# Kernel tuning notes

Hardware: AMD Instinct MI355X
Metric: run time of the kernel (lower is better)

## Reference

```python
import jax, jax.numpy as jnp
import numpy as np

# dims: B batch, T timesteps, V nodes, D in-features, C channels, d pos-emb dim,
# TS = t_size (spatio-temporal window), P prediction steps, L layers (=4, fixed by GLU(C*4))
B, T, V, D, C, d, TS, P, L = 4, 12, 512, 1, 64, 8, 3, 12, 4
BETA = TS - 1


def setup_inputs() -> dict:
    key = jax.random.key(0)
    ks = jax.random.split(key, 30)
    n = lambda i, shape, s=1.0: jax.random.normal(ks[i], shape, dtype=jnp.float32) * s
    return dict(
        x=n(0, (B, T, V, D)),
        sape=n(1, (V, d)),
        tape=n(2, (B, T, 1, d)),
        srpe=n(3, (V, V, d)),
        trpe=n(4, (TS, 1, d)),
        zeros_x=jnp.zeros((B, BETA, V, C), jnp.float32),
        zeros_tape=jnp.zeros((B, BETA, 1, d), jnp.float32),
        range_mask=(jax.random.uniform(ks[5], (B, V, TS * V)) < 0.5).astype(jnp.float32),
        Wi=n(6, (D, C), D ** -0.5), bi=n(7, (C,), 0.02),
        gc_mu=n(8, (L, 6, d)), gc_sig=n(9, (L, 6, d), 0.5),
        Wg=n(10, (L, C, 2 * C), C ** -0.5), bg=n(11, (L, 2 * C), 0.02),
        Wsp=n(12, (L, d, 2 * C), d ** -0.5), Wtp=n(13, (L, d, 2 * C), d ** -0.5),
        fs_w=n(14, (L, C, C, T), (C * T) ** -0.5), fs_b=n(15, (L, C), 0.02),
        glu1_w=n(16, (L, 2 * C, C), C ** -0.5), glu1_b=n(17, (L, 2 * C), 0.02),
        gout_w=n(18, (8 * C, 4 * C), (4 * C) ** -0.5), gout_b=n(19, (8 * C,), 0.02),
        out_w=n(20, (P, 4 * C), (4 * C) ** -0.5), out_b=n(21, (P,), 0.02),
    )


def _glu_cv(w, b, y):
    # 1x1-conv GLU over channel dim of y: (B, Cin, V) -> (B, Cin, V)
    z = jnp.einsum('oc,bcv->bov', w, y) + b[None, :, None]
    zl, zr = jnp.split(z, 2, axis=1)
    return zl * jax.nn.sigmoid(zr)


def _forward(x, sape, tape, srpe, trpe, Wi, bi, gc_mu, gc_sig, Wg, bg, Wsp, Wtp,
             fs_w, fs_b, glu1_w, glu1_b, gout_w, gout_b, out_w, out_b,
             zeros_x, zeros_tape, range_mask):
    b_, t_ = x.shape[0], x.shape[1]
    v_ = sape.shape[0]
    ts = trpe.shape[0]
    widx = jnp.arange(t_)[:, None] + jnp.arange(ts)  # (T, t_size) sliding-window indices
    h = x @ Wi + bi                                   # InputLayer: B,T,V,C
    tape_pad = jnp.concatenate([zeros_tape, tape], axis=1)  # B,T+beta,1,d
    skips = []
    for l in range(gc_mu.shape[0]):
        mu, sig = gc_mu[l], gc_sig[l]
        gc = lambda emb, i: jnp.sum(-0.5 * (emb - mu[i]) ** 2 * sig[i] ** 2, axis=-1)
        # STPRI: Gaussian position-aware relation inference
        base = gc(sape, 0)[:, None] + gc(sape, 1)[None, :] + gc(srpe, 4)        # (V_i, V_j)
        per_t = gc(tape, 2)[:, :, 0][:, :, None] \
              + gc(tape_pad, 3)[:, :, 0][:, widx] \
              + gc(trpe, 5)[:, 0]                                               # B,T,t_size
        S = jnp.exp(per_t[:, :, :, None, None] + base)                          # B,T,k,i,j (<=1, safe)
        S = S.transpose(0, 1, 4, 2, 3).reshape(b_, t_, v_, ts * v_)             # B,T,j,(k*V+i)
        S = S * range_mask[:, None]                                             # masked relations
        # STPGConv: masked graph conv over the t_size*V window + gating
        x_pad = jnp.concatenate([zeros_x, h], axis=1)                           # B,T+beta,V,C
        xw = x_pad[:, widx].reshape(b_, t_, ts * v_, -1)                        # B,T,t_size*V,C
        g = jnp.einsum('btjm,btmc->btjc', S, xw) @ Wg[l] + bg[l]                # B,T,V,2C
        g = g + sape @ Wsp[l] + tape @ Wtp[l]                                   # +SE(V,2C) +TE(B,T,1,2C)
        gl, gr = jnp.split(g, 2, axis=-1)
        h = gl * jax.nn.sigmoid(gr)                                             # B,T,V,C
        # GFS: conv over time (kernel (1,T)) + GLU -> B,C,V
        y = jnp.einsum('bcvt,oct->bov', h.transpose(0, 3, 2, 1), fs_w[l]) + fs_b[l][None, :, None]
        skips.append(_glu_cv(glu1_w[l], glu1_b[l], y))
    s = _glu_cv(gout_w, gout_b, jnp.concatenate(skips, axis=1))                  # B,4C,V
    return jnp.einsum('oc,bcv->bov', out_w, s) + out_b[None, :, None]            # B,P,V


def reference(x, sape, tape, srpe, trpe, zeros_x, zeros_tape, range_mask, Wi, bi,
              gc_mu, gc_sig, Wg, bg, Wsp, Wtp, fs_w, fs_b, glu1_w, glu1_b,
              gout_w, gout_b, out_w, out_b):
    return _forward(x, sape, tape, srpe, trpe, Wi, bi, gc_mu, gc_sig, Wg, bg, Wsp, Wtp,
                    fs_w, fs_b, glu1_w, glu1_b, gout_w, gout_b, out_w, out_b,
                    zeros_x, zeros_tape, range_mask)
```

## Files before the change

### kernel.cpp

```cpp
#include <hip/hip_runtime.h>
#include <math.h>


typedef unsigned short u16;
typedef __attribute__((ext_vector_type(8))) short short8;
typedef __attribute__((ext_vector_type(4))) float f32x4;
typedef __attribute__((ext_vector_type(8))) unsigned short u16x8;
typedef __attribute__((ext_vector_type(4))) unsigned short u16x4;

#define MFMA16(a, b, c) __builtin_amdgcn_mfma_f32_16x16x32_bf16((a), (b), (c), 0, 0, 0)

__device__ __forceinline__ float b2f(u16 u) {
  union { unsigned int i; float f; } x; x.i = ((unsigned int)u) << 16; return x.f;
}
__device__ __forceinline__ u16 f2b(float f) {
  union { float f; unsigned int i; } x; x.f = f;
  unsigned int r = x.i + 0x7FFFu + ((x.i >> 16) & 1u);
  return (u16)(r >> 16);
}
__device__ __forceinline__ void ld8f(const float* __restrict__ p, float* f) {
  f32x4 a = *(const f32x4*)p;
  f32x4 b = *(const f32x4*)(p + 4);
  #pragma unroll
  for (int i = 0; i < 4; ++i) { f[i] = a[i]; f[4 + i] = b[i]; }
}
__device__ __forceinline__ float gcf(const float* e, const float* __restrict__ mu,
                                     const float* __restrict__ sg) {
  float s = 0.f;
  #pragma unroll
  for (int i = 0; i < 8; ++i) {
    float dm = e[i] - mu[i];
    s += dm * dm * sg[i] * sg[i];
  }
  return -0.5f * s;
}
__device__ __forceinline__ float sigm(float v) { return 1.0f / (1.0f + expf(-v)); }

__global__ __launch_bounds__(256) void prep_kernel(
    const float* __restrict__ x, const float* __restrict__ sape,
    const float* __restrict__ tape, const float* __restrict__ srpe,
    const float* __restrict__ trpe, const float* __restrict__ Wi,
    const float* __restrict__ bi, const float* __restrict__ gmu,
    const float* __restrict__ gsg, const float* __restrict__ Wg,
    const float* __restrict__ bg, const float* __restrict__ Wsp,
    const float* __restrict__ Wtp, const float* __restrict__ fsw,
    const float* __restrict__ mask,
    const float* __restrict__ g1w, const float* __restrict__ gw,
    const float* __restrict__ ow,
    u16* __restrict__ hT0, u16* __restrict__ Abf,
    float* __restrict__ spb, float* __restrict__ tpb,
    u16* __restrict__ fswT, u16* __restrict__ WgT, float* __restrict__ ev,
    u16* __restrict__ g1wB, u16* __restrict__ gwB, u16* __restrict__ owB) {
  const int tid = threadIdx.x;
  int bid = blockIdx.x;

  if (bid < 768) {
    int gid = bid * 256 + tid;
    int i8 = gid & 63, c = (gid >> 6) & 63, bt = gid >> 12;
    float xv[8];
    ld8f(&x[bt * 512 + i8 * 8], xv);
    float wic = Wi[c], bic = bi[c];
    u16x8 hv;
    #pragma unroll
    for (int ii = 0; ii < 8; ++ii) hv[ii] = f2b(xv[ii] * wic + bic);
    *(u16x8*)&hT0[gid * 8] = hv;
    return;
  }
  bid -= 768;
  if (bid < 1024) {
    int gid = bid * 256 + tid;
    int i = gid & 511, j = gid >> 9;
    float fi[8], fj[8], fr[8];
    ld8f(sape + i * 8, fi);
    ld8f(sape + j * 8, fj);
    ld8f(srpe + ((size_t)i * 512 + j) * 8, fr);
    u16 eb[4];
    #pragma unroll
    for (int l = 0; l < 4; ++l) {
      const float* mub = gmu + l * 48;
      const float* sgb = gsg + l * 48;
      float s = gcf(fi, mub + 0, sgb + 0)
              + gcf(fj, mub + 8, sgb + 8)
              + gcf(fr, mub + 32, sgb + 32);
      eb[l] = f2b(expf(s));
    }
    #pragma unroll
    for (int b = 0; b < 4; ++b)
      #pragma unroll
      for (int k = 0; k < 3; ++k) {
        float mv = mask[((size_t)(b * 512 + j)) * 1536 + k * 512 + i];
        u16 m = (mv != 0.f) ? (u16)0xFFFFu : (u16)0;
        #pragma unroll
        for (int l = 0; l < 4; ++l)
          Abf[((size_t)((l * 4 + b) * 512 + j)) * 1536 + k * 512 + i] = eb[l] & m;
      }
    return;
  }
  bid -= 1024;
  if (bid < 1024) {
    int gid = bid * 256 + tid;
    int o = gid & 127, j = (gid >> 7) & 511, l = gid >> 16;
    float a = 0.f;
    #pragma unroll
    for (int dd = 0; dd < 8; ++dd)
      a += sape[j * 8 + dd] * Wsp[(l * 8 + dd) * 128 + o];
    spb[gid] = a;
    return;
  }
  bid -= 1024;
  if (bid < 96) {
    int gid = bid * 256 + tid;
    int o = gid & 127, bt = (gid >> 7) % 48, l = gid / 6144;
    float a = bg[l * 128 + o];
    #pragma unroll
    for (int dd = 0; dd < 8; ++dd)
      a += tape[bt * 8 + dd] * Wtp[(l * 8 + dd) * 128 + o];
    tpb[gid] = a;
    return;
  }
  bid -= 96;
  if (bid < 768) {
    int gid = bid * 256 + tid;
    int kidx = gid % 768, rest = gid / 768;
    int o = rest & 63, l = rest >> 6;
    int c = kidx & 63, tt = kidx >> 6;
    fswT[gid] = f2b(fsw[((l * 64 + o) * 64 + c) * 12 + tt]);
    return;
  }
  bid -= 768;
  if (bid < 128) {
    int gid = bid * 256 + tid;
    int c = gid & 63, o = (gid >> 6) & 127, l = gid >> 13;
    WgT[gid] = f2b(Wg[(l * 64 + c) * 128 + o]);
    return;
  }
  bid -= 128;
  if (bid < 3) {
    int gid = bid * 256 + tid;
    if (gid < 576) {
      int k = gid % 3, t = (gid / 3) % 12, b = (gid / 36) % 4, l = gid / 144;
      const float* mub = gmu + l * 48;
      const float* sgb = gsg + l * 48;
      float e2[8], e3[8], e5[8];
      ld8f(tape + (b * 12 + t) * 8, e2);
      int tp = t + k - 2;
      if (tp >= 0) ld8f(tape + (b * 12 + tp) * 8, e3);
      else {
        #pragma unroll
        for (int ii = 0; ii < 8; ++ii) e3[ii] = 0.f;
      }
      ld8f(trpe + k * 8, e5);
      float s = gcf(e2, mub + 16, sgb + 16)
              + gcf(e3, mub + 24, sgb + 24)
              + gcf(e5, mub + 40, sgb + 40);
      ev[gid] = expf(s);
    }
    return;
  }
  bid -= 3;
  if (bid < 128) {
    int gid = bid * 256 + tid;
    g1wB[gid] = f2b(g1w[gid]);
    return;
  }
  bid -= 128;
  if (bid < 512) {
    int gid = bid * 256 + tid;
    gwB[gid] = f2b(gw[gid]);
    return;
  }
  bid -= 512;
  {
    int gid = bid * 256 + tid;
    if (gid < 3072) owB[gid] = f2b(ow[gid]);
  }
}

__global__ __launch_bounds__(256) void agg_kernel(
    const u16* __restrict__ Abfl, const u16* __restrict__ hT,
    u16* __restrict__ G) {
  __shared__ u16 As[128][72];
  __shared__ u16 Bs[128][72];
  const int tid = threadIdx.x, wid = tid >> 6, lane = tid & 63;
  const int l16 = lane & 15, quad = lane >> 4;
  const int bid = blockIdx.x;
  const int nt = bid % 6;
  const int mt = (bid / 6) & 3;
  const int k  = (bid / 24) % 3;
  const int b  = bid / 72;
  const int wm = wid >> 1, wn = wid & 1;

  const u16* Arow0 = Abfl + ((size_t)(b * 512 + mt * 128)) * 1536 + k * 512;
  f32x4 acc[4][4] = {};

  for (int it = 0; it < 8; ++it) {
    const int i0 = it * 64;
    #pragma unroll
    for (int s = 0; s < 4; ++s) {
      int idx = s * 256 + tid;
      int r = idx >> 3, ch = (idx & 7) * 8;
      *(u16x8*)&As[r][ch] = *(const u16x8*)&Arow0[(size_t)r * 1536 + i0 + ch];
      int tp = nt * 2 + (r >> 6), c = r & 63;
      *(u16x8*)&Bs[r][ch] =
          *(const u16x8*)&hT[((size_t)((b * 12 + tp) * 64 + c)) * 512 + i0 + ch];
    }
    __syncthreads();
    #pragma unroll
    for (int ks = 0; ks < 2; ++ks) {
      short8 af[4], bf[4];
      #pragma unroll
      for (int mb = 0; mb < 4; ++mb)
        af[mb] = *(const short8*)&As[wm * 64 + mb * 16 + l16][ks * 32 + quad * 8];
      #pragma unroll
      for (int nb = 0; nb < 4; ++nb)
        bf[nb] = *(const short8*)&Bs[wn * 64 + nb * 16 + l16][ks * 32 + quad * 8];
      #pragma unroll
      for (int mb = 0; mb < 4; ++mb)
        #pragma unroll
        for (int nb = 0; nb < 4; ++nb)
          acc[mb][nb] = MFMA16(af[mb], bf[nb], acc[mb][nb]);
    }
    __syncthreads();
  }

  u16* Gp = G + ((size_t)((b * 3 + k) * 512 + mt * 128)) * 768 + nt * 128;
  #pragma unroll
  for (int mb = 0; mb < 4; ++mb)
    #pragma unroll
    for (int nb = 0; nb < 4; ++nb) {
      int n = wn * 64 + nb * 16 + l16;
      #pragma unroll
      for (int r = 0; r < 4; ++r) {
        int m = wm * 64 + mb * 16 + quad * 4 + r;
        Gp[(size_t)m * 768 + n] = f2b(acc[mb][nb][r]);
      }
    }
}

__global__ __launch_bounds__(256) void combine_kernel(
    const u16* __restrict__ G, const float* __restrict__ evl,
    const u16* __restrict__ WgTl, const float* __restrict__ spbl,
    const float* __restrict__ tpbl, const u16* __restrict__ fswTl,
    u16* __restrict__ hTout, float* __restrict__ ypl) {
  __shared__ u16 aggL[128][72];
  __shared__ u16 hL[128][72];
  const int tid = threadIdx.x, wid = tid >> 6, lane = tid & 63;
  const int l16 = lane & 15, quad = lane >> 4;
  const int bid = blockIdx.x;
  const int mt = bid & 3;
  const int bt = bid >> 2;
  const int b = bt / 12, t = bt - b * 12;

  {
    int j = tid >> 1;
    int c0 = (tid & 1) * 32;
    float accv[32];
    #pragma unroll
    for (int ii = 0; ii < 32; ++ii) accv[ii] = 0.f;
    #pragma unroll
    for (int k = 0; k < 3; ++k) {
      int tp = t + k - 2;
      if (tp < 0) continue;
      float ek = evl[bt * 3 + k];
      const u16* gp = &G[((size_t)((b * 3 + k) * 512 + mt * 128 + j)) * 768 + tp * 64 + c0];
      #pragma unroll
      for (int s = 0; s < 4; ++s) {
        u16x8 gv = *(const u16x8*)&gp[s * 8];
        #pragma unroll
        for (int ii = 0; ii < 8; ++ii) accv[s * 8 + ii] += b2f(gv[ii]) * ek;
      }
    }
    #pragma unroll
    for (int s = 0; s < 4; ++s) {
      u16x8 ov;
      #pragma unroll
      for (int ii = 0; ii < 8; ++ii) ov[ii] = f2b(accv[s * 8 + ii]);
      *(u16x8*)&aggL[j][c0 + s * 8] = ov;
    }
  }
  __syncthreads();

  f32x4 acc2[8][2] = {};
  #pragma unroll
  for (int ks = 0; ks < 2; ++ks) {
    short8 bf[2];
    #pragma unroll
    for (int nb = 0; nb < 2; ++nb)
      bf[nb] = *(const short8*)&aggL[wid * 32 + nb * 16 + l16][ks * 32 + quad * 8];
    #pragma unroll
    for (int mb = 0; mb < 8; ++mb) {
      short8 a = *(const short8*)&WgTl[(mb * 16 + l16) * 64 + ks * 32 + quad * 8];
      acc2[mb][0] = MFMA16(a, bf[0], acc2[mb][0]);
      acc2[mb][1] = MFMA16(a, bf[1], acc2[mb][1]);
    }
  }

  #pragma unroll
  for (int mb = 0; mb < 4; ++mb) {
    int ob = mb * 16 + quad * 4;
    #pragma unroll
    for (int nb = 0; nb < 2; ++nb) {
      int jl = wid * 32 + nb * 16 + l16;
      int jg = mt * 128 + jl;
      f32x4 spl = *(const f32x4*)&spbl[jg * 128 + ob];
      f32x4 spr = *(const f32x4*)&spbl[jg * 128 + 64 + ob];
      f32x4 tpl = *(const f32x4*)&tpbl[bt * 128 + ob];
      f32x4 tpr = *(const f32x4*)&tpbl[bt * 128 + 64 + ob];
      #pragma unroll
      for (int r = 0; r < 4; ++r) {
        float vl = acc2[mb][nb][r] + spl[r] + tpl[r];
        float vr = acc2[mb + 4][nb][r] + spr[r] + tpr[r];
        u16 hb = f2b(vl * sigm(vr));
        hTout[((size_t)((b * 12 + t) * 64 + ob + r)) * 512 + jg] = hb;
        hL[jl][ob + r] = hb;
      }
    }
  }
  __syncthreads();

  f32x4 accY[4][2] = {};
  #pragma unroll
  for (int ks = 0; ks < 2; ++ks) {
    short8 bfv[2];
    #pragma unroll
    for (int nb = 0; nb < 2; ++nb)
      bfv[nb] = *(const short8*)&hL[wid * 32 + nb * 16 + l16][ks * 32 + quad * 8];
    #pragma unroll
    for (int mb = 0; mb < 4; ++mb) {
      short8 a = *(const short8*)&fswTl[(mb * 16 + l16) * 768 + t * 64 + ks * 32 + quad * 8];
      accY[mb][0] = MFMA16(a, bfv[0], accY[mb][0]);
      accY[mb][1] = MFMA16(a, bfv[1], accY[mb][1]);
    }
  }
  #pragma unroll
  for (int mb = 0; mb < 4; ++mb)
    #pragma unroll
    for (int nb = 0; nb < 2; ++nb) {
      int j = mt * 128 + wid * 32 + nb * 16 + l16;
      #pragma unroll
      for (int r = 0; r < 4; ++r) {
        int o = mb * 16 + quad * 4 + r;
        ypl[((size_t)(bt * 64 + o)) * 512 + j] = accY[mb][nb][r];
      }
    }
}

__global__ __launch_bounds__(256) void final_kernel(
    const float* __restrict__ yp, const float* __restrict__ fsb,
    const u16* __restrict__ g1wB, const float* __restrict__ g1b,
    const u16* __restrict__ gwB, const float* __restrict__ gb,
    const u16* __restrict__ owB, const float* __restrict__ obv,
    float* __restrict__ out) {
  __shared__ u16 yL[64][72];
  __shared__ float zL[128][72];
  __shared__ u16 cL[64][264];
  __shared__ u16 sT[64][264];
  const int tid = threadIdx.x, wid = tid >> 6, lane = tid & 63;
  const int l16 = lane & 15, quad = lane >> 4;
  const int b = blockIdx.x >> 3;
  const int v0 = (blockIdx.x & 7) * 64;

  for (int l = 0; l < 4; ++l) {
    {
      int o = tid >> 2, vq = tid & 3;
      float fb = fsb[l * 64 + o];
      f32x4 sum[4];
      #pragma unroll
      for (int s = 0; s < 4; ++s)
        #pragma unroll
        for (int jj = 0; jj < 4; ++jj) sum[s][jj] = fb;
      for (int t = 0; t < 12; ++t) {
        const float* pp = &yp[(size_t)l * 1572864 +
                              ((size_t)((b * 12 + t) * 64 + o)) * 512 + v0 + vq * 16];
        #pragma unroll
        for (int s = 0; s < 4; ++s) {
          f32x4 v = *(const f32x4*)&pp[s * 4];
          sum[s] += v;
        }
      }
      #pragma unroll
      for (int s = 0; s < 4; ++s)
        #pragma unroll
        for (int jj = 0; jj < 4; ++jj)
          yL[vq * 16 + s * 4 + jj][o] = f2b(sum[s][jj]);
    }
    __syncthreads();
    f32x4 a1[2][4] = {};
    #pragma unroll
    for (int ks = 0; ks < 2; ++ks) {
      short8 bfv[4];
      #pragma unroll
      for (int nb = 0; nb < 4; ++nb)
        bfv[nb] = *(const short8*)&yL[nb * 16 + l16][ks * 32 + quad * 8];
      #pragma unroll
      for (int mb = 0; mb < 2; ++mb) {
        short8 a = *(const short8*)&g1wB[l * 8192 + (wid * 32 + mb * 16 + l16) * 64 +
                                         ks * 32 + quad * 8];
        #pragma unroll
        for (int nb = 0; nb < 4; ++nb) a1[mb][nb] = MFMA16(a, bfv[nb], a1[mb][nb]);
      }
    }
    #pragma unroll
    for (int mb = 0; mb < 2; ++mb)
      #pragma unroll
      for (int nb = 0; nb < 4; ++nb)
        #pragma unroll
        for (int r = 0; r < 4; ++r)
          zL[wid * 32 + mb * 16 + quad * 4 + r][nb * 16 + l16] = a1[mb][nb][r];
    __syncthreads();
    {
      int o = tid >> 2, vv0 = (tid & 3) * 16;
      float bl = g1b[l * 128 + o], br = g1b[l * 128 + 64 + o];
      #pragma unroll
      for (int ii = 0; ii < 16; ++ii) {
        float zl = zL[o][vv0 + ii] + bl;
        float zr = zL[o + 64][vv0 + ii] + br;
        cL[vv0 + ii][l * 64 + o] = f2b(zl * sigm(zr));
      }
    }
    __syncthreads();
  }

  f32x4 acc[8][4] = {};
  #pragma unroll
  for (int ks = 0; ks < 8; ++ks) {
    short8 bf[4];
    #pragma unroll
    for (int nb = 0; nb < 4; ++nb)
      bf[nb] = *(const short8*)&cL[nb * 16 + l16][ks * 32 + quad * 8];
    #pragma unroll
    for (int mb = 0; mb < 8; ++mb) {
      int og = (mb < 4 ? wid * 64 + mb * 16 : 256 + wid * 64 + (mb - 4) * 16) + l16;
      short8 a = *(const short8*)&gwB[og * 256 + ks * 32 + quad * 8];
      #pragma unroll
      for (int nb = 0; nb < 4; ++nb) acc[mb][nb] = MFMA16(a, bf[nb], acc[mb][nb]);
    }
  }
  #pragma unroll
  for (int mb = 0; mb < 4; ++mb)
    #pragma unroll
    for (int nb = 0; nb < 4; ++nb) {
      int vloc = nb * 16 + l16;
      int cc0 = wid * 64 + mb * 16 + quad * 4;
      u16x4 pk;
      #pragma unroll
      for (int r = 0; r < 4; ++r) {
        float zl = acc[mb][nb][r] + gb[cc0 + r];
        float zr = acc[mb + 4][nb][r] + gb[256 + cc0 + r];
        pk[r] = f2b(zl * sigm(zr));
      }
      *(u16x4*)&sT[vloc][cc0] = pk;
    }
  __syncthreads();

  f32x4 acc3 = {};
  #pragma unroll
  for (int ks = 0; ks < 8; ++ks) {
    short8 a;
    if (l16 < 12) a = *(const short8*)&owB[l16 * 256 + ks * 32 + quad * 8];
    else {
      #pragma unroll
      for (int ii = 0; ii < 8; ++ii) a[ii] = 0;
    }
    short8 bf = *(const short8*)&sT[wid * 16 + l16][ks * 32 + quad * 8];
    acc3 = MFMA16(a, bf, acc3);
  }
  #pragma unroll
  for (int r = 0; r < 4; ++r) {
    int p = quad * 4 + r;
    if (p < 12)
      out[(b * 12 + p) * 512 + v0 + wid * 16 + l16] = acc3[r] + obv[p];
  }
}

extern "C" void kernel_launch(void* const* d_in, const int* in_sizes, int n_in,
                              void* d_out, int out_size, void* d_ws, size_t ws_size,
                              hipStream_t stream) {
  const float* x    = (const float*)d_in[0];
  const float* sape = (const float*)d_in[1];
  const float* tape = (const float*)d_in[2];
  const float* srpe = (const float*)d_in[3];
  const float* trpe = (const float*)d_in[4];
  const float* mask = (const float*)d_in[7];
  const float* Wi   = (const float*)d_in[8];
  const float* bi   = (const float*)d_in[9];
  const float* gmu  = (const float*)d_in[10];
  const float* gsg  = (const float*)d_in[11];
  const float* Wg   = (const float*)d_in[12];
  const float* bg   = (const float*)d_in[13];
  const float* Wsp  = (const float*)d_in[14];
  const float* Wtp  = (const float*)d_in[15];
  const float* fsw  = (const float*)d_in[16];
  const float* fsb  = (const float*)d_in[17];
  const float* g1w  = (const float*)d_in[18];
  const float* g1b  = (const float*)d_in[19];
  const float* gow  = (const float*)d_in[20];
  const float* gob  = (const float*)d_in[21];
  const float* ow   = (const float*)d_in[22];
  const float* obv  = (const float*)d_in[23];

  char* w = (char*)d_ws;
  u16*   hT_a = (u16*)(w + 0);
  u16*   hT_b = (u16*)(w + 3145728);
  u16*   Abf  = (u16*)(w + 6291456);
  u16*   G    = (u16*)(w + 31457280);
  u16*   fswT = (u16*)(w + 40894464);
  u16*   WgT  = (u16*)(w + 41287680);
  u16*   g1wB = (u16*)(w + 41353216);
  u16*   gwB  = (u16*)(w + 41418752);
  u16*   owB  = (u16*)(w + 41680896);
  float* spb  = (float*)(w + 41689088);
  float* tpb  = (float*)(w + 42737664);
  float* ev   = (float*)(w + 42835968);
  float* yp   = (float*)(w + 42845184);

  prep_kernel<<<4463, 256, 0, stream>>>(x, sape, tape, srpe, trpe, Wi, bi, gmu, gsg,
                                        Wg, bg, Wsp, Wtp, fsw, mask, g1w, gow, ow,
                                        hT_a, Abf, spb, tpb, fswT, WgT, ev,
                                        g1wB, gwB, owB);
  u16* hin = hT_a;
  u16* hout = hT_b;
  for (int l = 0; l < 4; ++l) {
    agg_kernel<<<288, 256, 0, stream>>>(Abf + (size_t)l * 3145728, hin, G);
    combine_kernel<<<192, 256, 0, stream>>>(G, ev + l * 144, WgT + l * 8192,
                                            spb + l * 65536, tpb + l * 6144,
                                            fswT + l * 49152, hout,
                                            yp + (size_t)l * 1572864);
    u16* tmp = hin; hin = hout; hout = tmp;
  }
  final_kernel<<<32, 256, 0, stream>>>(yp, fsb, g1wB, g1b, gwB, gob, owB, obv,
                                       (float*)d_out);
}
```

Before: 274.4 us.

## Reduce GFS time-sum via atomics, prefetch agg tiles, stage G stores through LDS

The combine kernel now accumulates the per-timestep GFS conv partials straight into a zero-initialised (B,V,C) buffer with float atomicAdd. This replaces the old per-timestep yp buffer, which was written in full and then re-read and summed over time in the final kernel. The prep kernel gains blocks to zero that buffer, and the final kernel reads the reduced values directly. The agg kernel also register-prefetches the next K-tile during the MFMA loop, and stages its bf16 output through shared memory so global stores are coalesced. The atomics add contention over 12 timesteps and make the summation order nondeterministic.

Measured after the change: 343.9 us. +25.3%, slower.

```diff
diff --git a/kernel.cpp b/kernel.cpp
--- a/kernel.cpp
+++ b/kernel.cpp
@@ -50,7 +50,8 @@
     u16* __restrict__ hT0, u16* __restrict__ Abf,
     float* __restrict__ spb, float* __restrict__ tpb,
     u16* __restrict__ fswT, u16* __restrict__ WgT, float* __restrict__ ev,
-    u16* __restrict__ g1wB, u16* __restrict__ gwB, u16* __restrict__ owB) {
+    u16* __restrict__ g1wB, u16* __restrict__ gwB, u16* __restrict__ owB,
+    float* __restrict__ yF) {
   const int tid = threadIdx.x;
   int bid = blockIdx.x;
 
@@ -170,17 +171,23 @@
     return;
   }
   bid -= 512;
+  if (bid < 12) {
+    int gid = bid * 256 + tid;
+    if (gid < 3072) owB[gid] = f2b(ow[gid]);
+    return;
+  }
+  bid -= 12;
   {
     int gid = bid * 256 + tid;
-    if (gid < 3072) owB[gid] = f2b(ow[gid]);
+    f32x4 z = {0.f, 0.f, 0.f, 0.f};
+    *(f32x4*)&yF[gid * 4] = z;
   }
 }
 
 __global__ __launch_bounds__(256) void agg_kernel(
     const u16* __restrict__ Abfl, const u16* __restrict__ hT,
     u16* __restrict__ G) {
-  __shared__ u16 As[128][72];
-  __shared__ u16 Bs[128][72];
+  __shared__ u16 sm[2][128][72];
   const int tid = threadIdx.x, wid = tid >> 6, lane = tid & 63;
   const int l16 = lane & 15, quad = lane >> 4;
   const int bid = blockIdx.x;
@@ -193,27 +200,43 @@
   const u16* Arow0 = Abfl + ((size_t)(b * 512 + mt * 128)) * 1536 + k * 512;
   f32x4 acc[4][4] = {};
 
+  const int r0 = tid >> 3, ch0 = (tid & 7) * 8;
+  u16x8 ra[4], rb[4];
+  #pragma unroll
+  for (int s = 0; s < 4; ++s) {
+    int r = r0 + s * 32;
+    ra[s] = *(const u16x8*)&Arow0[(size_t)r * 1536 + ch0];
+    int tp = nt * 2 + (r >> 6), c = r & 63;
+    rb[s] = *(const u16x8*)&hT[((size_t)((b * 12 + tp) * 64 + c)) * 512 + ch0];
+  }
+
   for (int it = 0; it < 8; ++it) {
-    const int i0 = it * 64;
     #pragma unroll
     for (int s = 0; s < 4; ++s) {
-      int idx = s * 256 + tid;
-      int r = idx >> 3, ch = (idx & 7) * 8;
-      *(u16x8*)&As[r][ch] = *(const u16x8*)&Arow0[(size_t)r * 1536 + i0 + ch];
-      int tp = nt * 2 + (r >> 6), c = r & 63;
-      *(u16x8*)&Bs[r][ch] =
-          *(const u16x8*)&hT[((size_t)((b * 12 + tp) * 64 + c)) * 512 + i0 + ch];
+      int r = r0 + s * 32;
+      *(u16x8*)&sm[0][r][ch0] = ra[s];
+      *(u16x8*)&sm[1][r][ch0] = rb[s];
     }
     __syncthreads();
+    if (it < 7) {
+      int i0 = (it + 1) * 64;
+      #pragma unroll
+      for (int s = 0; s < 4; ++s) {
+        int r = r0 + s * 32;
+        ra[s] = *(const u16x8*)&Arow0[(size_t)r * 1536 + i0 + ch0];
+        int tp = nt * 2 + (r >> 6), c = r & 63;
+        rb[s] = *(const u16x8*)&hT[((size_t)((b * 12 + tp) * 64 + c)) * 512 + i0 + ch0];
+      }
+    }
     #pragma unroll
     for (int ks = 0; ks < 2; ++ks) {
       short8 af[4], bf[4];
       #pragma unroll
       for (int mb = 0; mb < 4; ++mb)
-        af[mb] = *(const short8*)&As[wm * 64 + mb * 16 + l16][ks * 32 + quad * 8];
+        af[mb] = *(const short8*)&sm[0][wm * 64 + mb * 16 + l16][ks * 32 + quad * 8];
       #pragma unroll
       for (int nb = 0; nb < 4; ++nb)
-        bf[nb] = *(const short8*)&Bs[wn * 64 + nb * 16 + l16][ks * 32 + quad * 8];
+        bf[nb] = *(const short8*)&sm[1][wn * 64 + nb * 16 + l16][ks * 32 + quad * 8];
       #pragma unroll
       for (int mb = 0; mb < 4; ++mb)
         #pragma unroll
@@ -223,7 +246,7 @@
     __syncthreads();
   }
 
-  u16* Gp = G + ((size_t)((b * 3 + k) * 512 + mt * 128)) * 768 + nt * 128;
+  u16* base = &sm[0][0][0];
   #pragma unroll
   for (int mb = 0; mb < 4; ++mb)
     #pragma unroll
@@ -232,16 +255,24 @@
       #pragma unroll
       for (int r = 0; r < 4; ++r) {
         int m = wm * 64 + mb * 16 + quad * 4 + r;
-        Gp[(size_t)m * 768 + n] = f2b(acc[mb][nb][r]);
-      }
-    }
+        base[m * 128 + n] = f2b(acc[mb][nb][r]);
+      }
+    }
+  __syncthreads();
+  u16* Gp = G + ((size_t)((b * 3 + k) * 512 + mt * 128)) * 768 + nt * 128;
+  #pragma unroll
+  for (int s = 0; s < 8; ++s) {
+    int idx = s * 256 + tid;
+    int m = idx >> 4, ch = (idx & 15) * 8;
+    *(u16x8*)&Gp[(size_t)m * 768 + ch] = *(const u16x8*)&base[m * 128 + ch];
+  }
 }
 
 __global__ __launch_bounds__(256) void combine_kernel(
     const u16* __restrict__ G, const float* __restrict__ evl,
     const u16* __restrict__ WgTl, const float* __restrict__ spbl,
     const float* __restrict__ tpbl, const u16* __restrict__ fswTl,
-    u16* __restrict__ hTout, float* __restrict__ ypl) {
+    u16* __restrict__ hTout, float* __restrict__ yFl) {
   __shared__ u16 aggL[128][72];
   __shared__ u16 hL[128][72];
   const int tid = threadIdx.x, wid = tid >> 6, lane = tid & 63;
@@ -337,16 +368,14 @@
     #pragma unroll
     for (int nb = 0; nb < 2; ++nb) {
       int j = mt * 128 + wid * 32 + nb * 16 + l16;
-      #pragma unroll
-      for (int r = 0; r < 4; ++r) {
-        int o = mb * 16 + quad * 4 + r;
-        ypl[((size_t)(bt * 64 + o)) * 512 + j] = accY[mb][nb][r];
-      }
+      float* yp = &yFl[((size_t)(b * 512 + j)) * 64 + mb * 16 + quad * 4];
+      #pragma unroll
+      for (int r = 0; r < 4; ++r) atomicAdd(&yp[r], accY[mb][nb][r]);
     }
 }
 
 __global__ __launch_bounds__(256) void final_kernel(
-    const float* __restrict__ yp, const float* __restrict__ fsb,
+    const float* __restrict__ yF, const float* __restrict__ fsb,
     const u16* __restrict__ g1wB, const float* __restrict__ g1b,
     const u16* __restrict__ gwB, const float* __restrict__ gb,
     const u16* __restrict__ owB, const float* __restrict__ obv,
@@ -362,27 +391,17 @@
 
   for (int l = 0; l < 4; ++l) {
     {
-      int o = tid >> 2, vq = tid & 3;
-      float fb = fsb[l * 64 + o];
-      f32x4 sum[4];
-      #pragma unroll
-      for (int s = 0; s < 4; ++s)
-        #pragma unroll
-        for (int jj = 0; jj < 4; ++jj) sum[s][jj] = fb;
-      for (int t = 0; t < 12; ++t) {
-        const float* pp = &yp[(size_t)l * 1572864 +
-                              ((size_t)((b * 12 + t) * 64 + o)) * 512 + v0 + vq * 16];
-        #pragma unroll
-        for (int s = 0; s < 4; ++s) {
-          f32x4 v = *(const f32x4*)&pp[s * 4];
-          sum[s] += v;
-        }
-      }
-      #pragma unroll
-      for (int s = 0; s < 4; ++s)
-        #pragma unroll
-        for (int jj = 0; jj < 4; ++jj)
-          yL[vq * 16 + s * 4 + jj][o] = f2b(sum[s][jj]);
+      int v = tid >> 2, o0 = (tid & 3) * 16;
+      const float* src = &yF[(size_t)l * 131072 + ((size_t)(b * 512 + v0 + v)) * 64 + o0];
+      #pragma unroll
+      for (int s = 0; s < 4; ++s) {
+        f32x4 vv = *(const f32x4*)&src[s * 4];
+        f32x4 fb = *(const f32x4*)&fsb[l * 64 + o0 + s * 4];
+        u16x4 pk;
+        #pragma unroll
+        for (int jj = 0; jj < 4; ++jj) pk[jj] = f2b(vv[jj] + fb[jj]);
+        *(u16x4*)&yL[v][o0 + s * 4] = pk;
+      }
     }
     __syncthreads();
     f32x4 a1[2][4] = {};
@@ -512,12 +531,12 @@
   float* spb  = (float*)(w + 41689088);
   float* tpb  = (float*)(w + 42737664);
   float* ev   = (float*)(w + 42835968);
-  float* yp   = (float*)(w + 42845184);
-
-  prep_kernel<<<4463, 256, 0, stream>>>(x, sape, tape, srpe, trpe, Wi, bi, gmu, gsg,
+  float* yF   = (float*)(w + 42852352);
+
+  prep_kernel<<<4975, 256, 0, stream>>>(x, sape, tape, srpe, trpe, Wi, bi, gmu, gsg,
                                         Wg, bg, Wsp, Wtp, fsw, mask, g1w, gow, ow,
                                         hT_a, Abf, spb, tpb, fswT, WgT, ev,
-                                        g1wB, gwB, owB);
+                                        g1wB, gwB, owB, yF);
   u16* hin = hT_a;
   u16* hout = hT_b;
   for (int l = 0; l < 4; ++l) {
@@ -525,9 +544,9 @@
     combine_kernel<<<192, 256, 0, stream>>>(G, ev + l * 144, WgT + l * 8192,
                                             spb + l * 65536, tpb + l * 6144,
                                             fswT + l * 49152, hout,
-                                            yp + (size_t)l * 1572864);
+                                            yF + (size_t)l * 131072);
     u16* tmp = hin; hin = hout; hout = tmp;
   }
-  final_kernel<<<32, 256, 0, stream>>>(yp, fsb, g1wB, g1b, gwB, gob, owB, obv,
+  final_kernel<<<32, 256, 0, stream>>>(yF, fsb, g1wB, g1b, gwB, gob, owB, obv,
                                        (float*)d_out);
 }
```
